# Performance work log

Measured on AMD Instinct MI355X. Metric: run time of the kernel, lower is better.

The kernel has to match this reference:

```python
import jax, jax.numpy as jnp
import numpy as np

N = 10000
H_INPUTS = 128
H = 512
RW_LEN = 16
BATCH = 512


def setup_inputs() -> dict:
    key = jax.random.key(0)
    ks = jax.random.split(key, 5)
    x = jax.random.normal(ks[0], (BATCH, RW_LEN, N + 1), dtype=jnp.float32)
    # xavier-ish scaled params
    W_down = jax.random.normal(ks[1], (N, H_INPUTS), dtype=jnp.float32) * (1.0 / np.sqrt(N))
    W_cell = jax.random.normal(ks[2], (H_INPUTS + 1 + H, 4 * H), dtype=jnp.float32) * (1.0 / np.sqrt(H_INPUTS + 1 + H))
    b_cell = jnp.zeros((4 * H,), dtype=jnp.float32)
    W_out = jax.random.normal(ks[3], (H, 1), dtype=jnp.float32) * (1.0 / np.sqrt(H))
    b_out = jnp.zeros((1,), dtype=jnp.float32)
    return {"x": x, "W_down": W_down, "W_cell": W_cell, "b_cell": b_cell,
            "W_out": W_out, "b_out": b_out}


def _forward(x, W_down, W_cell, b_cell, W_out, b_out):
    B = x.shape[0]
    x_rw = x[:, :, :N]                       # [B, T, N]
    x_weights = x[:, :, -1:]                 # [B, T, 1]
    xa = jnp.einsum('btn,nh->bth', x_rw, W_down)  # down-projection [B, T, H_in]
    xc = jnp.concatenate([xa, x_weights], axis=2)  # [B, T, H_in+1]
    xc_t = jnp.swapaxes(xc, 0, 1)            # [T, B, H_in+1] for scan

    h0 = jnp.zeros((B, H), dtype=x.dtype)
    c0 = jnp.zeros((B, H), dtype=x.dtype)

    def step(carry, xt):
        h, c = carry
        gates = jnp.concatenate([xt, h], axis=1) @ W_cell + b_cell  # [B, 4H]
        i_g, c_g, f_g, o_g = jnp.split(gates, 4, axis=1)
        # custom forget-gate bias of +1
        c_new = c * jax.nn.sigmoid(f_g + 1.0) + jax.nn.sigmoid(i_g) * jnp.tanh(c_g)
        h_new = jax.nn.sigmoid(o_g) * jnp.tanh(c_new)
        return (h_new, c_new), None

    (h, _), _ = jax.lax.scan(step, (h0, c0), xc_t)
    pred = h @ W_out + b_out                 # [B, 1]
    return pred


def reference(x, W_down, W_cell, b_cell, W_out, b_out):
    return _forward(x, W_down, W_cell, b_cell, W_out, b_out)
```

## Files before the change

kernel.cpp:

```cpp
#include <hip/hip_runtime.h>
#include <cmath>

#define TID ((int)threadIdx.x)

typedef __bf16 bf16_t;
typedef bf16_t bf16x8 __attribute__((ext_vector_type(8)));
typedef float floatx4 __attribute__((ext_vector_type(4)));

#define MFMA(a, b, c) __builtin_amdgcn_mfma_f32_16x16x32_bf16(a, b, c, 0, 0, 0)

constexpr int N_IN = 10000;
constexpr int XP   = 10001;
constexpr int KPD  = 10240;
constexpr int HH   = 512;
constexpr int TT   = 16;
constexpr int NB   = 512;
constexpr int MROW = 8192;
constexpr int KSPLIT = 16;
constexpr int KCHUNK = 640;
constexpr int KT_A = 10;

__device__ __forceinline__ float sigm(float x) { return 1.0f / (1.0f + expf(-x)); }

__device__ __forceinline__ void gload16(const void* g, void* lds) {
  __builtin_amdgcn_global_load_lds(
      (const __attribute__((address_space(1))) unsigned int*)g,
      (__attribute__((address_space(3))) unsigned int*)lds, 16, 0, 0);
}

__global__ __launch_bounds__(256)
void kPrepWd(const float* __restrict__ Wd, bf16_t* __restrict__ Whi, bf16_t* __restrict__ Wlo) {
  __shared__ float Ts[64][133];
  const int k0 = blockIdx.x * 64;
  #pragma unroll
  for (int i = 0; i < 32; ++i) {
    int f = TID + 256 * i;
    int kk = f >> 7, c = f & 127;
    int k = k0 + kk;
    Ts[kk][c] = (k < N_IN) ? Wd[(size_t)k * 128 + c] : 0.0f;
  }
  __syncthreads();
  const int lane = TID & 63, w = TID >> 6;
  for (int pass = 0; pass < 32; ++pass) {
    int c = pass * 4 + w;
    float v = Ts[lane][c];
    bf16_t hi = (bf16_t)v;
    bf16_t lo = (bf16_t)(v - (float)hi);
    Whi[(size_t)c * KPD + k0 + lane] = hi;
    Wlo[(size_t)c * KPD + k0 + lane] = lo;
  }
}

__global__ __launch_bounds__(256)
void kPrepWc(const float* __restrict__ Wc, bf16_t* __restrict__ Wxh, bf16_t* __restrict__ Wxl,
             float* __restrict__ wN, bf16_t* __restrict__ Whh, bf16_t* __restrict__ Whl) {
  __shared__ float Ts[64][133];
  const int k0 = blockIdx.x * 64;
  const int c0 = blockIdx.y * 128;
  #pragma unroll
  for (int i = 0; i < 32; ++i) {
    int f = TID + 256 * i;
    int kk = f >> 7, cc = f & 127;
    int k = k0 + kk;
    Ts[kk][cc] = (k < 641) ? Wc[(size_t)k * 2048 + c0 + cc] : 0.0f;
  }
  __syncthreads();
  const int lane = TID & 63, w = TID >> 6;
  const int k = k0 + lane;
  for (int pass = 0; pass < 32; ++pass) {
    int cc = pass * 4 + w;
    int c = c0 + cc;
    float v = Ts[lane][cc];
    bf16_t hi = (bf16_t)v;
    bf16_t lo = (bf16_t)(v - (float)hi);
    if (k < 128) {
      Wxh[(size_t)c * 128 + k] = hi;
      Wxl[(size_t)c * 128 + k] = lo;
    } else if (k == 128) {
      wN[c] = v;
    } else if (k < 641) {
      Whh[(size_t)c * 512 + (k - 129)] = hi;
      Whl[(size_t)c * 512 + (k - 129)] = lo;
    }
  }
}

__global__ __launch_bounds__(256)
void kPrepXw(const float* __restrict__ x, float* __restrict__ xw) {
  int r = blockIdx.x * 256 + TID;
  xw[r] = x[(size_t)r * XP + N_IN];
}

__global__ __launch_bounds__(256, 2)
void kA_mfma(const float* __restrict__ x, const bf16_t* __restrict__ Whi,
             const bf16_t* __restrict__ Wlo, float* __restrict__ parts) {
  __shared__ __align__(16) bf16_t Bt[2][2048 * 8];
  const int lane = TID & 63, w = TID >> 6;
  const int row0 = blockIdx.x * 128 + w * 32;
  const int kbase = blockIdx.y * KCHUNK;
  floatx4 acc[2][8] = {};

  auto STAGE = [&](int buf, int kt) {
    const int k0 = kbase + kt * 64;
    #pragma unroll
    for (int i = 0; i < 8; ++i) {
      int L = i * 256 + TID;
      int arr = L >> 10, col = (L >> 3) & 127, g = L & 7;
      int gs = g ^ (col & 7);
      const bf16_t* src = (arr ? Wlo : Whi) + (size_t)col * KPD + k0 + gs * 8;
      gload16(src, &Bt[buf][(size_t)L * 8]);
    }
  };
  auto LOADX = [&](float4 (&xb)[2][2][2], int kt) {
    const int k0 = kbase + kt * 64;
    #pragma unroll
    for (int rf = 0; rf < 2; ++rf) {
      const float* xp = x + (size_t)(row0 + rf * 16 + (lane & 15)) * XP;
      #pragma unroll
      for (int h = 0; h < 2; ++h) {
        int kk0 = k0 + h * 32 + (lane >> 4) * 8;
        if (kk0 < N_IN) {
          xb[rf][h][0] = *(const float4*)(xp + kk0);
          xb[rf][h][1] = *(const float4*)(xp + kk0 + 4);
        } else {
          xb[rf][h][0] = make_float4(0.f, 0.f, 0.f, 0.f);
          xb[rf][h][1] = make_float4(0.f, 0.f, 0.f, 0.f);
        }
      }
    }
  };
  auto COMPUTE = [&](int buf, const float4 (&xb)[2][2][2]) {
    #pragma unroll
    for (int h = 0; h < 2; ++h) {
      const int p = h * 4 + (lane >> 4);
      bf16x8 ahi[2], alo[2];
      #pragma unroll
      for (int rf = 0; rf < 2; ++rf) {
        float vv[8] = {xb[rf][h][0].x, xb[rf][h][0].y, xb[rf][h][0].z, xb[rf][h][0].w,
                       xb[rf][h][1].x, xb[rf][h][1].y, xb[rf][h][1].z, xb[rf][h][1].w};
        #pragma unroll
        for (int e = 0; e < 8; ++e) {
          bf16_t hi = (bf16_t)vv[e];
          ahi[rf][e] = hi;
          alo[rf][e] = (bf16_t)(vv[e] - (float)hi);
        }
      }
      #pragma unroll
      for (int cf = 0; cf < 8; ++cf) {
        const int col = cf * 16 + (lane & 15);
        const int g = p ^ (col & 7);
        bf16x8 bhi = *(const bf16x8*)&Bt[buf][(col * 8 + g) * 8];
        bf16x8 blo = *(const bf16x8*)&Bt[buf][(1024 + col * 8 + g) * 8];
        #pragma unroll
        for (int rf = 0; rf < 2; ++rf) {
          acc[rf][cf] = MFMA(ahi[rf], bhi, acc[rf][cf]);
          acc[rf][cf] = MFMA(ahi[rf], blo, acc[rf][cf]);
          acc[rf][cf] = MFMA(alo[rf], bhi, acc[rf][cf]);
        }
      }
    }
  };

  float4 xbA[2][2][2], xbB[2][2][2];
  STAGE(0, 0);
  LOADX(xbA, 0);
  __syncthreads();
  #pragma unroll
  for (int kt = 0; kt < KT_A; kt += 2) {
    if (kt + 1 < KT_A) { STAGE(1, kt + 1); LOADX(xbB, kt + 1); }
    COMPUTE(0, xbA);
    __syncthreads();
    if (kt + 2 < KT_A) { STAGE(0, kt + 2); LOADX(xbA, kt + 2); }
    COMPUTE(1, xbB);
    __syncthreads();
  }

  float* dst = parts + (size_t)blockIdx.y * MROW * 128;
  #pragma unroll
  for (int rf = 0; rf < 2; ++rf)
    #pragma unroll
    for (int cf = 0; cf < 8; ++cf)
      #pragma unroll
      for (int r = 0; r < 4; ++r) {
        int row = row0 + rf * 16 + (lane >> 4) * 4 + r;
        int col = cf * 16 + (lane & 15);
        dst[(size_t)row * 128 + col] = acc[rf][cf][r];
      }
}

__global__ __launch_bounds__(256)
void kRed(const float* __restrict__ parts, float* __restrict__ xa) {
  size_t i4 = ((size_t)blockIdx.x * 256 + TID) * 4;
  float4 v = make_float4(0.f, 0.f, 0.f, 0.f);
  #pragma unroll
  for (int s = 0; s < KSPLIT; ++s) {
    float4 p = *(const float4*)&parts[(size_t)s * MROW * 128 + i4];
    v.x += p.x; v.y += p.y; v.z += p.z; v.w += p.w;
  }
  *(float4*)&xa[i4] = v;
}

__global__ __launch_bounds__(512, 2)
void kGx(const float* __restrict__ xa, const float* __restrict__ xw,
         const bf16_t* __restrict__ Wxh, const bf16_t* __restrict__ Wxl,
         const float* __restrict__ wN, const float* __restrict__ bc,
         float* __restrict__ gx) {
  __shared__ __align__(16) bf16_t Bt[4096 * 8];
  const int lane = TID & 63, w = TID >> 6;
  const int wr = w & 3, wc = w >> 2;
  const int rowbase = blockIdx.x * 128 + wr * 32;
  const int JB = blockIdx.y * 32;
  floatx4 acc[2][4] = {};

  #pragma unroll
  for (int i = 0; i < 8; ++i) {
    int L = i * 512 + TID;
    int arr = L >> 11, ce = (L >> 4) & 127, g = L & 15;
    int gs = g ^ (ce & 15);
    int c_src = (ce & 3) * 512 + JB + (ce >> 2);
    const bf16_t* src = (arr ? Wxl : Wxh) + (size_t)c_src * 128 + gs * 8;
    gload16(src, &Bt[(size_t)L * 8]);
  }
  float4 xb[2][2][2][2];
  #pragma unroll
  for (int kt = 0; kt < 2; ++kt)
    #pragma unroll
    for (int rf = 0; rf < 2; ++rf) {
      const float* ap = xa + (size_t)(rowbase + rf * 16 + (lane & 15)) * 128;
      #pragma unroll
      for (int h = 0; h < 2; ++h) {
        int kk0 = kt * 64 + h * 32 + (lane >> 4) * 8;
        xb[kt][rf][h][0] = *(const float4*)(ap + kk0);
        xb[kt][rf][h][1] = *(const float4*)(ap + kk0 + 4);
      }
    }
  __syncthreads();
  #pragma unroll
  for (int kt = 0; kt < 2; ++kt) {
    #pragma unroll
    for (int h = 0; h < 2; ++h) {
      const int p = kt * 8 + h * 4 + (lane >> 4);
      bf16x8 ahi[2], alo[2];
      #pragma unroll
      for (int rf = 0; rf < 2; ++rf) {
        float vv[8] = {xb[kt][rf][h][0].x, xb[kt][rf][h][0].y, xb[kt][rf][h][0].z, xb[kt][rf][h][0].w,
                       xb[kt][rf][h][1].x, xb[kt][rf][h][1].y, xb[kt][rf][h][1].z, xb[kt][rf][h][1].w};
        #pragma unroll
        for (int e = 0; e < 8; ++e) {
          bf16_t hi = (bf16_t)vv[e];
          ahi[rf][e] = hi;
          alo[rf][e] = (bf16_t)(vv[e] - (float)hi);
        }
      }
      #pragma unroll
      for (int cf = 0; cf < 4; ++cf) {
        const int ce = wc * 64 + cf * 16 + (lane & 15);
        const int g = p ^ (ce & 15);
        bf16x8 bhi = *(const bf16x8*)&Bt[(ce * 16 + g) * 8];
        bf16x8 blo = *(const bf16x8*)&Bt[(2048 + ce * 16 + g) * 8];
        #pragma unroll
        for (int rf = 0; rf < 2; ++rf) {
          acc[rf][cf] = MFMA(ahi[rf], bhi, acc[rf][cf]);
          acc[rf][cf] = MFMA(ahi[rf], blo, acc[rf][cf]);
          acc[rf][cf] = MFMA(alo[rf], bhi, acc[rf][cf]);
        }
      }
    }
  }
  #pragma unroll
  for (int rf = 0; rf < 2; ++rf)
    #pragma unroll
    for (int cf = 0; cf < 4; ++cf) {
      const int ce = wc * 64 + cf * 16 + (lane & 15);
      const int n = blockIdx.y * 128 + ce;
      const int c_src = (ce & 3) * 512 + JB + (ce >> 2);
      const float bias = bc[c_src];
      const float wn = wN[c_src];
      #pragma unroll
      for (int r = 0; r < 4; ++r) {
        int row = rowbase + rf * 16 + (lane >> 4) * 4 + r;
        gx[(size_t)row * 2048 + n] = acc[rf][cf][r] + bias + xw[row] * wn;
      }
    }
}

__global__ __launch_bounds__(128, 2)
void kStepH(const bf16_t* __restrict__ hhi_in, const bf16_t* __restrict__ hlo_in,
            const bf16_t* __restrict__ Whh, const bf16_t* __restrict__ Whl,
            const float* __restrict__ gx, const float* __restrict__ c_in,
            bf16_t* __restrict__ hhi_out, bf16_t* __restrict__ hlo_out,
            float* __restrict__ c_out, int t, int has_h) {
  __shared__ __align__(16) bf16_t Bt[2][1024 * 8];
  const int lane = TID & 63, w = TID >> 6;
  const int j0 = blockIdx.x * 16;
  const int brow0 = blockIdx.y * 32 + w * 16;
  floatx4 acc[4] = {};

  auto STAGE = [&](int buf, int kt) {
    const int k0 = kt * 64;
    #pragma unroll
    for (int i = 0; i < 8; ++i) {
      int L = i * 128 + TID;
      int arr = L >> 9, ce = (L >> 3) & 63, g = L & 7;
      int gs = g ^ (ce & 7);
      int c_src = (ce >> 4) * 512 + j0 + (ce & 15);
      const bf16_t* src = (arr ? Whl : Whh) + (size_t)c_src * 512 + k0 + gs * 8;
      gload16(src, &Bt[buf][(size_t)L * 8]);
    }
  };
  auto LOADA = [&](bf16x8 (&ar)[2][2], int kt) {
    const int b = brow0 + (lane & 15);
    #pragma unroll
    for (int h = 0; h < 2; ++h) {
      const int kk0 = kt * 64 + h * 32 + (lane >> 4) * 8;
      ar[h][0] = *(const bf16x8*)&hhi_in[(size_t)b * HH + kk0];
      ar[h][1] = *(const bf16x8*)&hlo_in[(size_t)b * HH + kk0];
    }
  };
  auto COMPUTE = [&](int buf, const bf16x8 (&ar)[2][2]) {
    #pragma unroll
    for (int h = 0; h < 2; ++h) {
      const int p = h * 4 + (lane >> 4);
      #pragma unroll
      for (int cf = 0; cf < 4; ++cf) {
        const int ce = cf * 16 + (lane & 15);
        const int g = p ^ (ce & 7);
        bf16x8 bhi = *(const bf16x8*)&Bt[buf][(ce * 8 + g) * 8];
        bf16x8 blo = *(const bf16x8*)&Bt[buf][(512 + ce * 8 + g) * 8];
        acc[cf] = MFMA(ar[h][0], bhi, acc[cf]);
        acc[cf] = MFMA(ar[h][0], blo, acc[cf]);
        acc[cf] = MFMA(ar[h][1], bhi, acc[cf]);
      }
    }
  };

  if (has_h) {
    bf16x8 aA[2][2], aB[2][2];
    STAGE(0, 0);
    LOADA(aA, 0);
    __syncthreads();
    #pragma unroll
    for (int kt = 0; kt < 8; kt += 2) {
      if (kt + 1 < 8) { STAGE(1, kt + 1); LOADA(aB, kt + 1); }
      COMPUTE(0, aA);
      __syncthreads();
      if (kt + 2 < 8) { STAGE(0, kt + 2); LOADA(aA, kt + 2); }
      COMPUTE(1, aB);
      __syncthreads();
    }
  }

  const int j = j0 + (lane & 15);
  #pragma unroll
  for (int r = 0; r < 4; ++r) {
    int b = brow0 + (lane >> 4) * 4 + r;
    float4 gv = *(const float4*)&gx[((size_t)b * TT + t) * 2048 + (size_t)j * 4];
    float gi = acc[0][r] + gv.x;
    float gc = acc[1][r] + gv.y;
    float gf = acc[2][r] + gv.z;
    float go = acc[3][r] + gv.w;
    float cp = has_h ? c_in[(size_t)b * HH + j] : 0.0f;
    float cn = cp * sigm(gf + 1.0f) + sigm(gi) * tanhf(gc);
    float hn = sigm(go) * tanhf(cn);
    c_out[(size_t)b * HH + j] = cn;
    bf16_t hh = (bf16_t)hn;
    hhi_out[(size_t)b * HH + j] = hh;
    hlo_out[(size_t)b * HH + j] = (bf16_t)(hn - (float)hh);
  }
}

__global__ __launch_bounds__(64)
void kC_out(const bf16_t* __restrict__ hh, const bf16_t* __restrict__ hl,
            const float* __restrict__ Wo, const float* __restrict__ bo,
            float* __restrict__ out) {
  const int b = blockIdx.x;
  float s = 0.0f;
  for (int j = TID; j < HH; j += 64)
    s += ((float)hh[(size_t)b * HH + j] + (float)hl[(size_t)b * HH + j]) * Wo[j];
  #pragma unroll
  for (int off = 32; off > 0; off >>= 1) s += __shfl_down(s, off);
  if (TID == 0) out[b] = s + bo[0];
}

extern "C" void kernel_launch(void* const* d_in, const int* in_sizes, int n_in,
                              void* d_out, int out_size, void* d_ws, size_t ws_size,
                              hipStream_t stream) {
  const float* x  = (const float*)d_in[0];
  const float* Wd = (const float*)d_in[1];
  const float* Wc = (const float*)d_in[2];
  const float* bc = (const float*)d_in[3];
  const float* Wo = (const float*)d_in[4];
  const float* bo = (const float*)d_in[5];
  float* out = (float*)d_out;

  char* wsb = (char*)d_ws;
  size_t off = 0;
  auto alloc = [&](size_t bytes) -> void* {
    void* p = wsb + off;
    off = (off + bytes + 255) & ~(size_t)255;
    return p;
  };
  bf16_t* WdThi = (bf16_t*)alloc((size_t)128 * KPD * 2);
  bf16_t* WdTlo = (bf16_t*)alloc((size_t)128 * KPD * 2);
  bf16_t* WxThi = (bf16_t*)alloc((size_t)2048 * 128 * 2);
  bf16_t* WxTlo = (bf16_t*)alloc((size_t)2048 * 128 * 2);
  bf16_t* WhThi = (bf16_t*)alloc((size_t)2048 * 512 * 2);
  bf16_t* WhTlo = (bf16_t*)alloc((size_t)2048 * 512 * 2);
  float*  wN    = (float*)alloc(2048 * 4);
  float*  xw    = (float*)alloc(MROW * 4);
  float*  xa    = (float*)alloc((size_t)MROW * 128 * 4);
  float*  parts = (float*)alloc((size_t)KSPLIT * MROW * 128 * 4);
  float*  gx    = parts;
  bf16_t* h0hi = (bf16_t*)alloc((size_t)NB * HH * 2);
  bf16_t* h0lo = (bf16_t*)alloc((size_t)NB * HH * 2);
  bf16_t* h1hi = (bf16_t*)alloc((size_t)NB * HH * 2);
  bf16_t* h1lo = (bf16_t*)alloc((size_t)NB * HH * 2);
  float*  c0   = (float*)alloc((size_t)NB * HH * 4);
  float*  c1   = (float*)alloc((size_t)NB * HH * 4);
  bf16_t* hhi[2] = {h0hi, h1hi};
  bf16_t* hlo[2] = {h0lo, h1lo};
  float*  cb[2]  = {c0, c1};

  kPrepWd<<<160, 256, 0, stream>>>(Wd, WdThi, WdTlo);
  kPrepWc<<<dim3(11, 16), 256, 0, stream>>>(Wc, WxThi, WxTlo, wN, WhThi, WhTlo);
  kPrepXw<<<32, 256, 0, stream>>>(x, xw);
  kA_mfma<<<dim3(64, KSPLIT), 256, 0, stream>>>(x, WdThi, WdTlo, parts);
  kRed<<<1024, 256, 0, stream>>>(parts, xa);
  kGx<<<dim3(64, 16), 512, 0, stream>>>(xa, xw, WxThi, WxTlo, wN, bc, gx);
  for (int t = 0; t < TT; ++t) {
    kStepH<<<dim3(32, 16), 128, 0, stream>>>(hhi[t & 1], hlo[t & 1], WhThi, WhTlo,
        gx, cb[t & 1], hhi[(t + 1) & 1], hlo[(t + 1) & 1], cb[(t + 1) & 1],
        t, (t == 0) ? 0 : 1);
  }
  kC_out<<<512, 64, 0, stream>>>(h0hi, h0lo, Wo, bo, out);
}
```

Measured before the change: 403.3 us.

## Pre-pack W_down into MFMA fragment order and drop LDS staging in down-projection

The weight-prep kernel now writes W_down hi/lo bf16 parts directly in per-lane MFMA B-fragment order, so the down-projection kernel loads each B fragment straight from global memory into registers instead of staging through double-buffered LDS with barriers. The software pipelining of x loads and the barriers are removed. The kPrepXw launch is also dropped: the gate-input kernel reads the x weight column directly from x. The risk is that global loads are no longer overlapped with compute and that B fragments are re-fetched from L2 by every block instead of being shared through LDS.

```diff
diff --git a/kernel.cpp b/kernel.cpp
--- a/kernel.cpp
+++ b/kernel.cpp
@@ -29,7 +29,7 @@
 }
 
 __global__ __launch_bounds__(256)
-void kPrepWd(const float* __restrict__ Wd, bf16_t* __restrict__ Whi, bf16_t* __restrict__ Wlo) {
+void kPrepWd(const float* __restrict__ Wd, bf16_t* __restrict__ Phi, bf16_t* __restrict__ Plo) {
   __shared__ float Ts[64][133];
   const int k0 = blockIdx.x * 64;
   #pragma unroll
@@ -41,13 +41,24 @@
   }
   __syncthreads();
   const int lane = TID & 63, w = TID >> 6;
-  for (int pass = 0; pass < 32; ++pass) {
-    int c = pass * 4 + w;
-    float v = Ts[lane][c];
-    bf16_t hi = (bf16_t)v;
-    bf16_t lo = (bf16_t)(v - (float)hi);
-    Whi[(size_t)c * KPD + k0 + lane] = hi;
-    Wlo[(size_t)c * KPD + k0 + lane] = lo;
+  const int p = lane >> 4, cl = lane & 15;
+  #pragma unroll
+  for (int i = 0; i < 2; ++i) {
+    int cf = w * 2 + i;
+    #pragma unroll
+    for (int h = 0; h < 2; ++h) {
+      bf16x8 hi8, lo8;
+      #pragma unroll
+      for (int e = 0; e < 8; ++e) {
+        float v = Ts[h * 32 + p * 8 + e][cf * 16 + cl];
+        bf16_t hi = (bf16_t)v;
+        hi8[e] = hi;
+        lo8[e] = (bf16_t)(v - (float)hi);
+      }
+      size_t base = ((((size_t)blockIdx.x * 8 + cf) * 2 + h) * 64 + lane) * 8;
+      *(bf16x8*)&Phi[base] = hi8;
+      *(bf16x8*)&Plo[base] = lo8;
+    }
   }
 }
 
@@ -85,34 +96,19 @@
   }
 }
 
-__global__ __launch_bounds__(256)
-void kPrepXw(const float* __restrict__ x, float* __restrict__ xw) {
-  int r = blockIdx.x * 256 + TID;
-  xw[r] = x[(size_t)r * XP + N_IN];
-}
-
 __global__ __launch_bounds__(256, 2)
-void kA_mfma(const float* __restrict__ x, const bf16_t* __restrict__ Whi,
-             const bf16_t* __restrict__ Wlo, float* __restrict__ parts) {
-  __shared__ __align__(16) bf16_t Bt[2][2048 * 8];
+void kA_mfma(const float* __restrict__ x, const bf16_t* __restrict__ Phi,
+             const bf16_t* __restrict__ Plo, float* __restrict__ parts) {
   const int lane = TID & 63, w = TID >> 6;
   const int row0 = blockIdx.x * 128 + w * 32;
   const int kbase = blockIdx.y * KCHUNK;
+  const int cbase = kbase >> 6;
   floatx4 acc[2][8] = {};
 
-  auto STAGE = [&](int buf, int kt) {
+  #pragma unroll 1
+  for (int kt = 0; kt < KT_A; ++kt) {
     const int k0 = kbase + kt * 64;
-    #pragma unroll
-    for (int i = 0; i < 8; ++i) {
-      int L = i * 256 + TID;
-      int arr = L >> 10, col = (L >> 3) & 127, g = L & 7;
-      int gs = g ^ (col & 7);
-      const bf16_t* src = (arr ? Wlo : Whi) + (size_t)col * KPD + k0 + gs * 8;
-      gload16(src, &Bt[buf][(size_t)L * 8]);
-    }
-  };
-  auto LOADX = [&](float4 (&xb)[2][2][2], int kt) {
-    const int k0 = kbase + kt * 64;
+    float4 xb[2][2][2];
     #pragma unroll
     for (int rf = 0; rf < 2; ++rf) {
       const float* xp = x + (size_t)(row0 + rf * 16 + (lane & 15)) * XP;
@@ -128,11 +124,15 @@
         }
       }
     }
-  };
-  auto COMPUTE = [&](int buf, const float4 (&xb)[2][2][2]) {
     #pragma unroll
     for (int h = 0; h < 2; ++h) {
-      const int p = h * 4 + (lane >> 4);
+      bf16x8 bh[8], bl[8];
+      #pragma unroll
+      for (int cf = 0; cf < 8; ++cf) {
+        size_t base = ((((size_t)(cbase + kt) * 8 + cf) * 2 + h) * 64 + lane) * 8;
+        bh[cf] = *(const bf16x8*)&Phi[base];
+        bl[cf] = *(const bf16x8*)&Plo[base];
+      }
       bf16x8 ahi[2], alo[2];
       #pragma unroll
       for (int rf = 0; rf < 2; ++rf) {
@@ -146,33 +146,14 @@
         }
       }
       #pragma unroll
-      for (int cf = 0; cf < 8; ++cf) {
-        const int col = cf * 16 + (lane & 15);
-        const int g = p ^ (col & 7);
-        bf16x8 bhi = *(const bf16x8*)&Bt[buf][(col * 8 + g) * 8];
-        bf16x8 blo = *(const bf16x8*)&Bt[buf][(1024 + col * 8 + g) * 8];
+      for (int cf = 0; cf < 8; ++cf)
         #pragma unroll
         for (int rf = 0; rf < 2; ++rf) {
-          acc[rf][cf] = MFMA(ahi[rf], bhi, acc[rf][cf]);
-          acc[rf][cf] = MFMA(ahi[rf], blo, acc[rf][cf]);
-          acc[rf][cf] = MFMA(alo[rf], bhi, acc[rf][cf]);
+          acc[rf][cf] = MFMA(ahi[rf], bh[cf], acc[rf][cf]);
+          acc[rf][cf] = MFMA(ahi[rf], bl[cf], acc[rf][cf]);
+          acc[rf][cf] = MFMA(alo[rf], bh[cf], acc[rf][cf]);
         }
-      }
-    }
-  };
-
-  float4 xbA[2][2][2], xbB[2][2][2];
-  STAGE(0, 0);
-  LOADX(xbA, 0);
-  __syncthreads();
-  #pragma unroll
-  for (int kt = 0; kt < KT_A; kt += 2) {
-    if (kt + 1 < KT_A) { STAGE(1, kt + 1); LOADX(xbB, kt + 1); }
-    COMPUTE(0, xbA);
-    __syncthreads();
-    if (kt + 2 < KT_A) { STAGE(0, kt + 2); LOADX(xbA, kt + 2); }
-    COMPUTE(1, xbB);
-    __syncthreads();
+    }
   }
 
   float* dst = parts + (size_t)blockIdx.y * MROW * 128;
@@ -201,7 +182,7 @@
 }
 
 __global__ __launch_bounds__(512, 2)
-void kGx(const float* __restrict__ xa, const float* __restrict__ xw,
+void kGx(const float* __restrict__ xa, const float* __restrict__ x,
          const bf16_t* __restrict__ Wxh, const bf16_t* __restrict__ Wxl,
          const float* __restrict__ wN, const float* __restrict__ bc,
          float* __restrict__ gx) {
@@ -279,7 +260,8 @@
       #pragma unroll
       for (int r = 0; r < 4; ++r) {
         int row = rowbase + rf * 16 + (lane >> 4) * 4 + r;
-        gx[(size_t)row * 2048 + n] = acc[rf][cf][r] + bias + xw[row] * wn;
+        float xwv = x[(size_t)row * XP + N_IN];
+        gx[(size_t)row * 2048 + n] = acc[rf][cf][r] + bias + xwv * wn;
       }
     }
 }
@@ -400,14 +382,13 @@
     off = (off + bytes + 255) & ~(size_t)255;
     return p;
   };
-  bf16_t* WdThi = (bf16_t*)alloc((size_t)128 * KPD * 2);
-  bf16_t* WdTlo = (bf16_t*)alloc((size_t)128 * KPD * 2);
+  bf16_t* WdPhi = (bf16_t*)alloc((size_t)128 * KPD * 2);
+  bf16_t* WdPlo = (bf16_t*)alloc((size_t)128 * KPD * 2);
   bf16_t* WxThi = (bf16_t*)alloc((size_t)2048 * 128 * 2);
   bf16_t* WxTlo = (bf16_t*)alloc((size_t)2048 * 128 * 2);
   bf16_t* WhThi = (bf16_t*)alloc((size_t)2048 * 512 * 2);
   bf16_t* WhTlo = (bf16_t*)alloc((size_t)2048 * 512 * 2);
   float*  wN    = (float*)alloc(2048 * 4);
-  float*  xw    = (float*)alloc(MROW * 4);
   float*  xa    = (float*)alloc((size_t)MROW * 128 * 4);
   float*  parts = (float*)alloc((size_t)KSPLIT * MROW * 128 * 4);
   float*  gx    = parts;
@@ -421,12 +402,11 @@
   bf16_t* hlo[2] = {h0lo, h1lo};
   float*  cb[2]  = {c0, c1};
 
-  kPrepWd<<<160, 256, 0, stream>>>(Wd, WdThi, WdTlo);
+  kPrepWd<<<160, 256, 0, stream>>>(Wd, WdPhi, WdPlo);
   kPrepWc<<<dim3(11, 16), 256, 0, stream>>>(Wc, WxThi, WxTlo, wN, WhThi, WhTlo);
-  kPrepXw<<<32, 256, 0, stream>>>(x, xw);
-  kA_mfma<<<dim3(64, KSPLIT), 256, 0, stream>>>(x, WdThi, WdTlo, parts);
+  kA_mfma<<<dim3(64, KSPLIT), 256, 0, stream>>>(x, WdPhi, WdPlo, parts);
   kRed<<<1024, 256, 0, stream>>>(parts, xa);
-  kGx<<<dim3(64, 16), 512, 0, stream>>>(xa, xw, WxThi, WxTlo, wN, bc, gx);
+  kGx<<<dim3(64, 16), 512, 0, stream>>>(xa, x, WxThi, WxTlo, wN, bc, gx);
   for (int t = 0; t < TT; ++t) {
     kStepH<<<dim3(32, 16), 128, 0, stream>>>(hhi[t & 1], hlo[t & 1], WhThi, WhTlo,
         gx, cb[t & 1], hhi[(t + 1) & 1], hlo[(t + 1) & 1], cb[(t + 1) & 1],
```

New measurement: 433.5 us. +7.5%, slower.

## Pre-pack recurrent weights into MFMA fragment order and drop LDS staging in step kernel

Applied to the files above, without the earlier changes.

Adds a one-time pack kernel that reorders the hi/lo recurrent weight matrices into per-lane MFMA B-fragment order. The per-timestep kernel can then read B operands straight from global memory with contiguous 16-byte loads, with no LDS double buffering or barriers. The tiny kPrepXw launch is also folded into kGx, which now reads the x weight column directly. The trade-off is losing LDS reuse of weights across the block's two waves, so each wave fetches the weights itself and relies on L2, plus extra workspace for the packed copies.

```diff
diff --git a/kernel.cpp b/kernel.cpp
--- a/kernel.cpp
+++ b/kernel.cpp
@@ -86,9 +86,18 @@
 }
 
 __global__ __launch_bounds__(256)
-void kPrepXw(const float* __restrict__ x, float* __restrict__ xw) {
-  int r = blockIdx.x * 256 + TID;
-  xw[r] = x[(size_t)r * XP + N_IN];
+void kPackWh(const bf16_t* __restrict__ Whh, const bf16_t* __restrict__ Whl,
+             bf16_t* __restrict__ Ph, bf16_t* __restrict__ Pl) {
+  const int lane = TID & 63, w = TID >> 6;
+  const int wid = blockIdx.x * 4 + w;
+  const int jt = wid >> 6, kt = (wid >> 3) & 7, h = (wid >> 2) & 1, cf = wid & 3;
+  const int p = lane >> 4, cl = lane & 15;
+  const int c = cf * 512 + jt * 16 + cl;
+  const size_t soff = (size_t)c * 512 + kt * 64 + h * 32 + p * 8;
+  bf16x8 hi8 = *(const bf16x8*)&Whh[soff];
+  bf16x8 lo8 = *(const bf16x8*)&Whl[soff];
+  *(bf16x8*)&Ph[(size_t)wid * 512 + lane * 8] = hi8;
+  *(bf16x8*)&Pl[(size_t)wid * 512 + lane * 8] = lo8;
 }
 
 __global__ __launch_bounds__(256, 2)
@@ -201,7 +210,7 @@
 }
 
 __global__ __launch_bounds__(512, 2)
-void kGx(const float* __restrict__ xa, const float* __restrict__ xw,
+void kGx(const float* __restrict__ xa, const float* __restrict__ x,
          const bf16_t* __restrict__ Wxh, const bf16_t* __restrict__ Wxl,
          const float* __restrict__ wN, const float* __restrict__ bc,
          float* __restrict__ gx) {
@@ -279,78 +288,50 @@
       #pragma unroll
       for (int r = 0; r < 4; ++r) {
         int row = rowbase + rf * 16 + (lane >> 4) * 4 + r;
-        gx[(size_t)row * 2048 + n] = acc[rf][cf][r] + bias + xw[row] * wn;
-      }
-    }
-}
-
-__global__ __launch_bounds__(128, 2)
-void kStepH(const bf16_t* __restrict__ hhi_in, const bf16_t* __restrict__ hlo_in,
-            const bf16_t* __restrict__ Whh, const bf16_t* __restrict__ Whl,
+        float xwv = x[(size_t)row * XP + N_IN];
+        gx[(size_t)row * 2048 + n] = acc[rf][cf][r] + bias + xwv * wn;
+      }
+    }
+}
+
+__global__ __launch_bounds__(128)
+void kStepP(const bf16_t* __restrict__ hhi_in, const bf16_t* __restrict__ hlo_in,
+            const bf16_t* __restrict__ Ph, const bf16_t* __restrict__ Pl,
             const float* __restrict__ gx, const float* __restrict__ c_in,
             bf16_t* __restrict__ hhi_out, bf16_t* __restrict__ hlo_out,
             float* __restrict__ c_out, int t, int has_h) {
-  __shared__ __align__(16) bf16_t Bt[2][1024 * 8];
-  const int lane = TID & 63, w = TID >> 6;
-  const int j0 = blockIdx.x * 16;
+  const int lane = TID & 63, w = TID >> 6;
+  const int jt = blockIdx.x;
   const int brow0 = blockIdx.y * 32 + w * 16;
   floatx4 acc[4] = {};
 
-  auto STAGE = [&](int buf, int kt) {
-    const int k0 = kt * 64;
-    #pragma unroll
-    for (int i = 0; i < 8; ++i) {
-      int L = i * 128 + TID;
-      int arr = L >> 9, ce = (L >> 3) & 63, g = L & 7;
-      int gs = g ^ (ce & 7);
-      int c_src = (ce >> 4) * 512 + j0 + (ce & 15);
-      const bf16_t* src = (arr ? Whl : Whh) + (size_t)c_src * 512 + k0 + gs * 8;
-      gload16(src, &Bt[buf][(size_t)L * 8]);
-    }
-  };
-  auto LOADA = [&](bf16x8 (&ar)[2][2], int kt) {
+  if (has_h) {
     const int b = brow0 + (lane & 15);
     #pragma unroll
-    for (int h = 0; h < 2; ++h) {
-      const int kk0 = kt * 64 + h * 32 + (lane >> 4) * 8;
-      ar[h][0] = *(const bf16x8*)&hhi_in[(size_t)b * HH + kk0];
-      ar[h][1] = *(const bf16x8*)&hlo_in[(size_t)b * HH + kk0];
-    }
-  };
-  auto COMPUTE = [&](int buf, const bf16x8 (&ar)[2][2]) {
-    #pragma unroll
-    for (int h = 0; h < 2; ++h) {
-      const int p = h * 4 + (lane >> 4);
-      #pragma unroll
-      for (int cf = 0; cf < 4; ++cf) {
-        const int ce = cf * 16 + (lane & 15);
-        const int g = p ^ (ce & 7);
-        bf16x8 bhi = *(const bf16x8*)&Bt[buf][(ce * 8 + g) * 8];
-        bf16x8 blo = *(const bf16x8*)&Bt[buf][(512 + ce * 8 + g) * 8];
-        acc[cf] = MFMA(ar[h][0], bhi, acc[cf]);
-        acc[cf] = MFMA(ar[h][0], blo, acc[cf]);
-        acc[cf] = MFMA(ar[h][1], bhi, acc[cf]);
-      }
-    }
-  };
-
-  if (has_h) {
-    bf16x8 aA[2][2], aB[2][2];
-    STAGE(0, 0);
-    LOADA(aA, 0);
-    __syncthreads();
-    #pragma unroll
-    for (int kt = 0; kt < 8; kt += 2) {
-      if (kt + 1 < 8) { STAGE(1, kt + 1); LOADA(aB, kt + 1); }
-      COMPUTE(0, aA);
-      __syncthreads();
-      if (kt + 2 < 8) { STAGE(0, kt + 2); LOADA(aA, kt + 2); }
-      COMPUTE(1, aB);
-      __syncthreads();
-    }
-  }
-
-  const int j = j0 + (lane & 15);
+    for (int kt = 0; kt < 8; ++kt) {
+      bf16x8 ar[2][2];
+      #pragma unroll
+      for (int h = 0; h < 2; ++h) {
+        const int kk0 = kt * 64 + h * 32 + (lane >> 4) * 8;
+        ar[h][0] = *(const bf16x8*)&hhi_in[(size_t)b * HH + kk0];
+        ar[h][1] = *(const bf16x8*)&hlo_in[(size_t)b * HH + kk0];
+      }
+      #pragma unroll
+      for (int h = 0; h < 2; ++h) {
+        #pragma unroll
+        for (int cf = 0; cf < 4; ++cf) {
+          const size_t base = (size_t)(((jt * 8 + kt) * 2 + h) * 4 + cf) * 512 + lane * 8;
+          bf16x8 bh = *(const bf16x8*)&Ph[base];
+          bf16x8 bl = *(const bf16x8*)&Pl[base];
+          acc[cf] = MFMA(ar[h][0], bh, acc[cf]);
+          acc[cf] = MFMA(ar[h][0], bl, acc[cf]);
+          acc[cf] = MFMA(ar[h][1], bh, acc[cf]);
+        }
+      }
+    }
+  }
+
+  const int j = jt * 16 + (lane & 15);
   #pragma unroll
   for (int r = 0; r < 4; ++r) {
     int b = brow0 + (lane >> 4) * 4 + r;
@@ -406,8 +387,9 @@
   bf16_t* WxTlo = (bf16_t*)alloc((size_t)2048 * 128 * 2);
   bf16_t* WhThi = (bf16_t*)alloc((size_t)2048 * 512 * 2);
   bf16_t* WhTlo = (bf16_t*)alloc((size_t)2048 * 512 * 2);
+  bf16_t* Ph    = (bf16_t*)alloc((size_t)2048 * 512 * 2);
+  bf16_t* Pl    = (bf16_t*)alloc((size_t)2048 * 512 * 2);
   float*  wN    = (float*)alloc(2048 * 4);
-  float*  xw    = (float*)alloc(MROW * 4);
   float*  xa    = (float*)alloc((size_t)MROW * 128 * 4);
   float*  parts = (float*)alloc((size_t)KSPLIT * MROW * 128 * 4);
   float*  gx    = parts;
@@ -423,12 +405,12 @@
 
   kPrepWd<<<160, 256, 0, stream>>>(Wd, WdThi, WdTlo);
   kPrepWc<<<dim3(11, 16), 256, 0, stream>>>(Wc, WxThi, WxTlo, wN, WhThi, WhTlo);
-  kPrepXw<<<32, 256, 0, stream>>>(x, xw);
+  kPackWh<<<512, 256, 0, stream>>>(WhThi, WhTlo, Ph, Pl);
   kA_mfma<<<dim3(64, KSPLIT), 256, 0, stream>>>(x, WdThi, WdTlo, parts);
   kRed<<<1024, 256, 0, stream>>>(parts, xa);
-  kGx<<<dim3(64, 16), 512, 0, stream>>>(xa, xw, WxThi, WxTlo, wN, bc, gx);
+  kGx<<<dim3(64, 16), 512, 0, stream>>>(xa, x, WxThi, WxTlo, wN, bc, gx);
   for (int t = 0; t < TT; ++t) {
-    kStepH<<<dim3(32, 16), 128, 0, stream>>>(hhi[t & 1], hlo[t & 1], WhThi, WhTlo,
+    kStepP<<<dim3(32, 16), 128, 0, stream>>>(hhi[t & 1], hlo[t & 1], Ph, Pl,
         gx, cb[t & 1], hhi[(t + 1) & 1], hlo[(t + 1) & 1], cb[(t + 1) & 1],
         t, (t == 0) ? 0 : 1);
   }
```

Measured after the change: 487.4 us. 20.8% more time.

## Use partial vmcnt waits in double-buffered loops and fold x-weight read into kGx

Applied to the files above, without the earlier changes.

Replaces the full __syncthreads in the kA_mfma and kStepH double-buffered loops with explicit s_waitcnt vmcnt(N) plus barrier, so the prefetch for the next tile can stay in flight while the current tile is computed. The x loads in kA_mfma become unconditional with clamped addresses and zeroing afterwards, which removes a branch around the loads. The kPrepXw kernel is dropped and kGx reads the last column of x directly, saving one launch at the cost of strided scalar loads inside kGx. The hand-written vmcnt counts must match the real number of outstanding loads, otherwise the code reads LDS or registers before the data has arrived.

```diff
diff --git a/kernel.cpp b/kernel.cpp
--- a/kernel.cpp
+++ b/kernel.cpp
@@ -8,6 +8,12 @@
 typedef float floatx4 __attribute__((ext_vector_type(4)));
 
 #define MFMA(a, b, c) __builtin_amdgcn_mfma_f32_16x16x32_bf16(a, b, c, 0, 0, 0)
+#define WAIT_BAR(N)  do { asm volatile("s_waitcnt vmcnt(" #N ")" ::: "memory"); \
+                          __builtin_amdgcn_s_barrier(); \
+                          __builtin_amdgcn_sched_barrier(0); } while (0)
+#define LGKM_BAR     do { asm volatile("s_waitcnt lgkmcnt(0)" ::: "memory"); \
+                          __builtin_amdgcn_s_barrier(); \
+                          __builtin_amdgcn_sched_barrier(0); } while (0)
 
 constexpr int N_IN = 10000;
 constexpr int XP   = 10001;
@@ -85,12 +91,6 @@
   }
 }
 
-__global__ __launch_bounds__(256)
-void kPrepXw(const float* __restrict__ x, float* __restrict__ xw) {
-  int r = blockIdx.x * 256 + TID;
-  xw[r] = x[(size_t)r * XP + N_IN];
-}
-
 __global__ __launch_bounds__(256, 2)
 void kA_mfma(const float* __restrict__ x, const bf16_t* __restrict__ Whi,
              const bf16_t* __restrict__ Wlo, float* __restrict__ parts) {
@@ -119,13 +119,15 @@
       #pragma unroll
       for (int h = 0; h < 2; ++h) {
         int kk0 = k0 + h * 32 + (lane >> 4) * 8;
-        if (kk0 < N_IN) {
-          xb[rf][h][0] = *(const float4*)(xp + kk0);
-          xb[rf][h][1] = *(const float4*)(xp + kk0 + 4);
-        } else {
-          xb[rf][h][0] = make_float4(0.f, 0.f, 0.f, 0.f);
-          xb[rf][h][1] = make_float4(0.f, 0.f, 0.f, 0.f);
+        int kc = (kk0 < N_IN) ? kk0 : (N_IN - 8);
+        float4 v0 = *(const float4*)(xp + kc);
+        float4 v1 = *(const float4*)(xp + kc + 4);
+        if (kk0 >= N_IN) {
+          v0 = make_float4(0.f, 0.f, 0.f, 0.f);
+          v1 = make_float4(0.f, 0.f, 0.f, 0.f);
         }
+        xb[rf][h][0] = v0;
+        xb[rf][h][1] = v1;
       }
     }
   };
@@ -164,15 +166,24 @@
   float4 xbA[2][2][2], xbB[2][2][2];
   STAGE(0, 0);
   LOADX(xbA, 0);
-  __syncthreads();
   #pragma unroll
   for (int kt = 0; kt < KT_A; kt += 2) {
-    if (kt + 1 < KT_A) { STAGE(1, kt + 1); LOADX(xbB, kt + 1); }
+    if (kt + 1 < KT_A) {
+      STAGE(1, kt + 1); LOADX(xbB, kt + 1);
+      WAIT_BAR(16);
+    } else {
+      WAIT_BAR(0);
+    }
     COMPUTE(0, xbA);
-    __syncthreads();
-    if (kt + 2 < KT_A) { STAGE(0, kt + 2); LOADX(xbA, kt + 2); }
+    LGKM_BAR;
+    if (kt + 2 < KT_A) {
+      STAGE(0, kt + 2); LOADX(xbA, kt + 2);
+      WAIT_BAR(16);
+    } else {
+      WAIT_BAR(0);
+    }
     COMPUTE(1, xbB);
-    __syncthreads();
+    LGKM_BAR;
   }
 
   float* dst = parts + (size_t)blockIdx.y * MROW * 128;
@@ -201,7 +212,7 @@
 }
 
 __global__ __launch_bounds__(512, 2)
-void kGx(const float* __restrict__ xa, const float* __restrict__ xw,
+void kGx(const float* __restrict__ xa, const float* __restrict__ x,
          const bf16_t* __restrict__ Wxh, const bf16_t* __restrict__ Wxl,
          const float* __restrict__ wN, const float* __restrict__ bc,
          float* __restrict__ gx) {
@@ -279,7 +290,8 @@
       #pragma unroll
       for (int r = 0; r < 4; ++r) {
         int row = rowbase + rf * 16 + (lane >> 4) * 4 + r;
-        gx[(size_t)row * 2048 + n] = acc[rf][cf][r] + bias + xw[row] * wn;
+        float xwv = x[(size_t)row * XP + N_IN];
+        gx[(size_t)row * 2048 + n] = acc[rf][cf][r] + bias + xwv * wn;
       }
     }
 }
@@ -338,15 +350,24 @@
     bf16x8 aA[2][2], aB[2][2];
     STAGE(0, 0);
     LOADA(aA, 0);
-    __syncthreads();
     #pragma unroll
     for (int kt = 0; kt < 8; kt += 2) {
-      if (kt + 1 < 8) { STAGE(1, kt + 1); LOADA(aB, kt + 1); }
+      if (kt + 1 < 8) {
+        STAGE(1, kt + 1); LOADA(aB, kt + 1);
+        WAIT_BAR(12);
+      } else {
+        WAIT_BAR(0);
+      }
       COMPUTE(0, aA);
-      __syncthreads();
-      if (kt + 2 < 8) { STAGE(0, kt + 2); LOADA(aA, kt + 2); }
+      LGKM_BAR;
+      if (kt + 2 < 8) {
+        STAGE(0, kt + 2); LOADA(aA, kt + 2);
+        WAIT_BAR(12);
+      } else {
+        WAIT_BAR(0);
+      }
       COMPUTE(1, aB);
-      __syncthreads();
+      LGKM_BAR;
     }
   }
 
@@ -407,7 +428,6 @@
   bf16_t* WhThi = (bf16_t*)alloc((size_t)2048 * 512 * 2);
   bf16_t* WhTlo = (bf16_t*)alloc((size_t)2048 * 512 * 2);
   float*  wN    = (float*)alloc(2048 * 4);
-  float*  xw    = (float*)alloc(MROW * 4);
   float*  xa    = (float*)alloc((size_t)MROW * 128 * 4);
   float*  parts = (float*)alloc((size_t)KSPLIT * MROW * 128 * 4);
   float*  gx    = parts;
@@ -423,10 +443,9 @@
 
   kPrepWd<<<160, 256, 0, stream>>>(Wd, WdThi, WdTlo);
   kPrepWc<<<dim3(11, 16), 256, 0, stream>>>(Wc, WxThi, WxTlo, wN, WhThi, WhTlo);
-  kPrepXw<<<32, 256, 0, stream>>>(x, xw);
   kA_mfma<<<dim3(64, KSPLIT), 256, 0, stream>>>(x, WdThi, WdTlo, parts);
   kRed<<<1024, 256, 0, stream>>>(parts, xa);
-  kGx<<<dim3(64, 16), 512, 0, stream>>>(xa, xw, WxThi, WxTlo, wN, bc, gx);
+  kGx<<<dim3(64, 16), 512, 0, stream>>>(xa, x, WxThi, WxTlo, wN, bc, gx);
   for (int t = 0; t < TT; ++t) {
     kStepH<<<dim3(32, 16), 128, 0, stream>>>(hhi[t & 1], hlo[t & 1], WhThi, WhTlo,
         gx, cb[t & 1], hhi[(t + 1) & 1], hlo[(t + 1) & 1], cb[(t + 1) & 1],
```

New measurement: 401.5 us. About the same (-0.5%).
